# Performance work log

Measured on AMD Instinct MI355X. Metric: run time of the kernel, lower is better.

The kernel has to match this reference:

```python
import jax, jax.numpy as jnp
import numpy as np
import math

NEG_INF = -10000.0

def setup_inputs() -> dict:
    key = jax.random.key(0)
    k1, k2, k3 = jax.random.split(key, 3)
    B, Sq, Sk, H, D = 2, 2048, 2048, 16, 64
    q = jax.random.normal(k1, (B, Sq, H, D), dtype=jnp.float32)
    kv = jax.random.normal(k2, (B, Sk, 2, H, D), dtype=jnp.float32)
    key_padding_mask = jax.random.randint(k3, (B, Sk), 0, 2).astype(jnp.bool_)
    return {"q": q, "kv": kv, "key_padding_mask": key_padding_mask}

def reference(q, kv, key_padding_mask):
    # q: (B, Sq, H, D); kv: (B, Sk, 2, H, D); key_padding_mask: (B, Sk) True=keep
    D = q.shape[-1]
    softmax_scale = 1.0 / math.sqrt(D)
    k = kv[:, :, 0]  # (B, Sk, H, D)
    v = kv[:, :, 1]  # (B, Sk, H, D)
    # (B, H, Sq, Sk) score matrix
    scores = jnp.einsum('bthd,bshd->bhts', q, k * softmax_scale)
    # additive padding mask: 0 where keep, NEG_INF where masked out
    pad = jnp.where(key_padding_mask, 0.0, NEG_INF).astype(scores.dtype)
    scores = scores + pad[:, None, None, :]
    attention = jax.nn.softmax(scores, axis=-1)
    # dropout_p = 0.0 (eval mode) -> no-op
    output = jnp.einsum('bhts,bshd->bthd', attention, v)
    return output
```

## Files before the change

kernel.cpp:

```cpp
#include <hip/hip_runtime.h>

typedef unsigned short u16;
typedef unsigned int   u32;
typedef u16   u16x8 __attribute__((ext_vector_type(8)));
typedef float f32x4 __attribute__((ext_vector_type(4)));
typedef float f32x16 __attribute__((ext_vector_type(16)));
typedef __bf16 bf16x8 __attribute__((ext_vector_type(8)));
typedef u32   u32x4 __attribute__((ext_vector_type(4)));

#define QSCALE  0.18033688011112f
#define BM_OPEN  -28.8539008177793f
#define BM_MASK  -14455.8043097f

__device__ __forceinline__ u16 f2bf(float x){
  __bf16 h = (__bf16)x;
  return __builtin_bit_cast(u16, h);
}
__device__ __forceinline__ f32x16 mfma32(u16x8 a, u16x8 b, f32x16 c){
  return __builtin_amdgcn_mfma_f32_32x32x16_bf16(
      __builtin_bit_cast(bf16x8, a), __builtin_bit_cast(bf16x8, b), c, 0, 0, 0);
}
__device__ __forceinline__ void gld16(const void* g, void* l){
  __builtin_amdgcn_global_load_lds(
      (const __attribute__((address_space(1))) u32*)g,
      (__attribute__((address_space(3))) u32*)l, 16, 0, 0);
}
__device__ __forceinline__ u32 cvtpk(float lo, float hi){
  u32 d;
  asm("v_cvt_pk_bf16_f32 %0, %1, %2" : "=v"(d) : "v"(lo), "v"(hi));
  return d;
}
__device__ __forceinline__ void plswap(u32 &x, u32 &y){
  asm("v_permlane32_swap_b32 %0, %1" : "+v"(x), "+v"(y));
}


__global__ __launch_bounds__(256, 4)
void prepass(const float* __restrict__ KV, const int* __restrict__ MASK,
             u16* __restrict__ IMG, float* __restrict__ BIASM)
{
  const int tid = threadIdx.x;
  const int bid = blockIdx.x;
  const int kt = bid & 31;
  const int h  = (bid >> 5) & 15;
  const int b  = bid >> 9;
  const int kb = kt*64;
  const size_t kv_b = (size_t)b*(2048u*2048u);
  u16* tile = IMG + (size_t)bid * 8192;

  {
    const int skey = tid >> 2, scp = tid & 3;
    const float* kp = KV + kv_b + (size_t)(kb + skey)*2048 + h*64 + 16*scp;
    f32x4 f0 = *(const f32x4*)(kp);
    f32x4 f1 = *(const f32x4*)(kp + 4);
    f32x4 f2 = *(const f32x4*)(kp + 8);
    f32x4 f3 = *(const f32x4*)(kp + 12);
    u16x8 c0, c1;
    #pragma unroll
    for (int e = 0; e < 4; ++e){
      c0[e] = f2bf(f0[e]); c0[e+4] = f2bf(f1[e]);
      c1[e] = f2bf(f2[e]); c1[e+4] = f2bf(f3[e]);
    }
    const int idx0 = skey*64 + (((2*scp) ^ (skey & 7)) << 3);
    *(u16x8*)&tile[idx0]     = c0;
    *(u16x8*)&tile[idx0 ^ 8] = c1;
  }
  {
    const int sdb = tid & 7, ssp = tid >> 3;
    const float* vp = KV + kv_b + (size_t)(kb + 2*ssp)*2048 + 1024 + h*64 + 8*sdb;
    f32x4 r0a = *(const f32x4*)(vp);
    f32x4 r0b = *(const f32x4*)(vp + 4);
    f32x4 r1a = *(const f32x4*)(vp + 2048);
    f32x4 r1b = *(const f32x4*)(vp + 2048 + 4);
    u32* vimg = (u32*)(tile + 4096);
    const int wc = ssp >> 2, wi = ssp & 3;
    #pragma unroll
    for (int j = 0; j < 4; ++j){
      const int d0 = 8*sdb + j;
      const int d1 = d0 + 4;
      vimg[d0*32 + ((wc ^ (d0 & 7)) << 2) + wi] = (u32)f2bf(r0a[j]) | ((u32)f2bf(r1a[j]) << 16);
      vimg[d1*32 + ((wc ^ (d1 & 7)) << 2) + wi] = (u32)f2bf(r0b[j]) | ((u32)f2bf(r1b[j]) << 16);
    }
  }
  if (h == 0 && tid < 64){
    const int s = kb + tid;
    BIASM[b*2048 + s] = MASK[b*2048 + s] ? BM_OPEN : BM_MASK;
  }
}

template<int PRE>
__global__ __launch_bounds__(256, 3)
void attn_main(const float* __restrict__ Q, const float* __restrict__ KV,
               const int* __restrict__ MASK, const u16* __restrict__ IMG,
               const float* __restrict__ BIASM, float* __restrict__ OUT)
{
  __shared__ __align__(16) u16 KVbuf[2][8192];
  __shared__ __align__(16) float BiasLds[2048];

  const int tid  = threadIdx.x;
  const int lane = tid & 63;
  const int hi   = lane >> 5;
  const int lq   = lane & 31;

  const int bid0 = blockIdx.x;
  const int bid  = (bid0 & 7)*64 + (bid0 >> 3);
  const int qt  = bid & 15;
  const int h   = (bid >> 4) & 15;
  const int b   = bid >> 8;

  const int w    = tid >> 6;
  const int qbase = qt*128 + w*32;
  const size_t q_b  = (size_t)b * (2048u*1024u);
  const size_t kv_b = (size_t)b * (2048u*2048u);

  const int sw7 = lq & 7;

  u16x8 Qf[4];
  {
    const int qrow = qbase + lq;
    const float* qp = Q + q_b + (size_t)qrow*1024 + h*64 + 8*hi;
    #pragma unroll
    for (int kc = 0; kc < 4; ++kc){
      f32x4 a = *(const f32x4*)(qp + 16*kc);
      f32x4 c = *(const f32x4*)(qp + 16*kc + 4);
      u16x8 v;
      #pragma unroll
      for (int e = 0; e < 4; ++e){
        v[e]     = f2bf(a[e] * QSCALE);
        v[e + 4] = f2bf(c[e] * QSCALE);
      }
      Qf[kc] = v;
    }
  }

  f32x16 Oa[2];
  #pragma unroll
  for (int dt = 0; dt < 2; ++dt)
    #pragma unroll
    for (int r = 0; r < 16; ++r) Oa[dt][r] = 0.f;
  float lrun = 0.f;

  const char* img0 = (const char*)IMG + (size_t)((b*16 + h)*32) * 16384;
  const int so = tid*16;
  const int skey = tid >> 2, scp = tid & 3;
  const int sdb  = tid & 7,  ssp = tid >> 3;
  const float* kp0 = KV + kv_b + (size_t)skey*2048 + h*64 + 16*scp;
  const float* vp0 = KV + kv_b + (size_t)(2*ssp)*2048 + 1024 + h*64 + 8*sdb;
  f32x4 kf0, kf1, kf2, kf3, va, vb2, vc, vd;

#define STAGE_ISSUE(T, DST) do{                                               \
    const char* g_ = img0 + (size_t)(T)*16384;                                \
    char* l_ = (char*)(DST);                                                  \
    gld16(g_+so,        l_+so);                                               \
    gld16(g_+so+4096,   l_+so+4096);                                          \
    gld16(g_+so+8192,   l_+so+8192);                                          \
    gld16(g_+so+12288,  l_+so+12288);                                         \
  }while(0)

#define BIAS_STAGE() do{                                                      \
    const char* gb_ = (const char*)BIASM + (size_t)b*8192;                    \
    char* lb_ = (char*)BiasLds;                                               \
    gld16(gb_+so,      lb_+so);                                               \
    gld16(gb_+so+4096, lb_+so+4096);                                          \
  }while(0)

#define STAGE_REG(T) do{                                                      \
    const float* kp_ = kp0 + (size_t)(T)*64*2048;                             \
    kf0=*(const f32x4*)(kp_);   kf1=*(const f32x4*)(kp_+4);                   \
    kf2=*(const f32x4*)(kp_+8); kf3=*(const f32x4*)(kp_+12);                  \
    const float* vp_ = vp0 + (size_t)(T)*64*2048;                             \
    va=*(const f32x4*)(vp_);      vb2=*(const f32x4*)(vp_+4);                 \
    vc=*(const f32x4*)(vp_+2048); vd =*(const f32x4*)(vp_+2048+4);            \
  }while(0)

#define STAGE_WRITE(DST) do{                                                  \
    u16x8 c0_, c1_;                                                           \
    _Pragma("unroll") for (int e_=0; e_<4; ++e_){                             \
      c0_[e_]=f2bf(kf0[e_]); c0_[e_+4]=f2bf(kf1[e_]);                         \
      c1_[e_]=f2bf(kf2[e_]); c1_[e_+4]=f2bf(kf3[e_]); }                       \
    const int kix_ = skey*64 + (((2*scp) ^ (skey & 7)) << 3);                 \
    *(u16x8*)&(DST)[kix_]     = c0_;                                          \
    *(u16x8*)&(DST)[kix_ ^ 8] = c1_;                                          \
    u32* vimg_ = (u32*)((DST)+4096);                                          \
    const int wc_ = ssp >> 2, wi_ = ssp & 3;                                  \
    _Pragma("unroll") for (int j_=0; j_<4; ++j_){                             \
      const int d0_=8*sdb+j_, d1_=d0_+4;                                      \
      vimg_[d0_*32 + ((wc_ ^ (d0_&7)) << 2) + wi_] = (u32)f2bf(va[j_])  | ((u32)f2bf(vc[j_])<<16); \
      vimg_[d1_*32 + ((wc_ ^ (d1_&7)) << 2) + wi_] = (u32)f2bf(vb2[j_]) | ((u32)f2bf(vd[j_])<<16); \
    }                                                                         \
  }while(0)

#define COMPUTE(T, CUR) do{                                                   \
    const u16* Kb_ = (CUR);                                                   \
    const u32* vimg_ = (const u32*)((CUR) + 4096);                            \
    f32x16 S[2];                                                              \
    _Pragma("unroll") for (int ct = 0; ct < 2; ++ct){                         \
      _Pragma("unroll") for (int m = 0; m < 4; ++m){                          \
        f32x4 bq;                                                             \
        if constexpr (PRE){                                                   \
          bq = *(const f32x4*)&BiasLds[(T)*64 + 32*ct + 8*m + 4*hi];          \
        } else {                                                              \
          const int4 mv = *(const int4*)(MASK + b*2048 + (T)*64 + 32*ct + 8*m + 4*hi); \
          bq[0] = mv.x ? BM_OPEN : BM_MASK;                                   \
          bq[1] = mv.y ? BM_OPEN : BM_MASK;                                   \
          bq[2] = mv.z ? BM_OPEN : BM_MASK;                                   \
          bq[3] = mv.w ? BM_OPEN : BM_MASK;                                   \
        }                                                                     \
        S[ct][4*m+0] = bq[0]; S[ct][4*m+1] = bq[1];                           \
        S[ct][4*m+2] = bq[2]; S[ct][4*m+3] = bq[3];                           \
      }                                                                       \
    }                                                                         \
    __builtin_amdgcn_s_setprio(1);                                            \
    _Pragma("unroll") for (int ct = 0; ct < 2; ++ct){                         \
      _Pragma("unroll") for (int kc = 0; kc < 4; ++kc){                       \
        u16x8 kf = *(const u16x8*)&Kb_[(32*ct + lq)*64 + (((2*kc+hi)^sw7)<<3)]; \
        S[ct] = mfma32(kf, Qf[kc], S[ct]);                                    \
      }                                                                       \
    }                                                                         \
    __builtin_amdgcn_s_setprio(0);                                            \
    u32 pa[2][4], pb[2][4];                                                   \
    float ps = 0.f;                                                           \
    _Pragma("unroll") for (int ct = 0; ct < 2; ++ct){                         \
      _Pragma("unroll") for (int m = 0; m < 4; ++m){                          \
        const float p0 = __builtin_amdgcn_exp2f(S[ct][4*m+0]);                \
        const float p1 = __builtin_amdgcn_exp2f(S[ct][4*m+1]);                \
        const float p2 = __builtin_amdgcn_exp2f(S[ct][4*m+2]);                \
        const float p3 = __builtin_amdgcn_exp2f(S[ct][4*m+3]);                \
        ps += (p0 + p1) + (p2 + p3);                                          \
        pa[ct][m] = cvtpk(p0, p1);                                            \
        pb[ct][m] = cvtpk(p2, p3);                                            \
      }                                                                       \
    }                                                                         \
    lrun += ps;                                                               \
    u16x8 Pf[4];                                                              \
    _Pragma("unroll") for (int ct = 0; ct < 2; ++ct){                         \
      plswap(pa[ct][0], pa[ct][1]);  plswap(pb[ct][0], pb[ct][1]);            \
      plswap(pa[ct][2], pa[ct][3]);  plswap(pb[ct][2], pb[ct][3]);            \
      u32x4 f0_ = { pa[ct][0], pb[ct][0], pa[ct][1], pb[ct][1] };             \
      u32x4 f1_ = { pa[ct][2], pb[ct][2], pa[ct][3], pb[ct][3] };             \
      Pf[2*ct+0] = __builtin_bit_cast(u16x8, f0_);                            \
      Pf[2*ct+1] = __builtin_bit_cast(u16x8, f1_);                            \
    }                                                                         \
    __builtin_amdgcn_s_setprio(1);                                            \
    _Pragma("unroll") for (int dt = 0; dt < 2; ++dt){                         \
      _Pragma("unroll") for (int sc = 0; sc < 4; ++sc){                       \
        u32x4 vv = *(const u32x4*)&vimg_[(32*dt + lq)*32 + (((2*sc+hi)^sw7)<<2)]; \
        Oa[dt] = mfma32(__builtin_bit_cast(u16x8, vv), Pf[sc], Oa[dt]);       \
      }                                                                       \
    }                                                                         \
    __builtin_amdgcn_s_setprio(0);                                            \
  }while(0)

  if constexpr (PRE){
    BIAS_STAGE();
    STAGE_ISSUE(0, &KVbuf[0][0]);
  } else {
    STAGE_REG(0);
    STAGE_WRITE(&KVbuf[0][0]);
  }
  __syncthreads();

  for (int t = 0; t < 32; ++t){
    if (t < 31){
      if constexpr (PRE) STAGE_ISSUE(t+1, &KVbuf[(t+1) & 1][0]);
      else               STAGE_REG(t+1);
    }
    COMPUTE(t, &KVbuf[t & 1][0]);
    if (t < 31){
      if constexpr (!PRE) STAGE_WRITE(&KVbuf[(t+1) & 1][0]);
      __syncthreads();
    }
  }

  {
    float l_ = lrun + __shfl_xor(lrun, 32, 64);
    const float inv = 1.f / l_;
    const int qrow = qbase + lq;
    float* op = OUT + q_b + (size_t)qrow*1024 + h*64;
    #pragma unroll
    for (int dt = 0; dt < 2; ++dt){
      #pragma unroll
      for (int m = 0; m < 4; ++m){
        f32x4 ov;
        ov[0] = Oa[dt][4*m+0] * inv;
        ov[1] = Oa[dt][4*m+1] * inv;
        ov[2] = Oa[dt][4*m+2] * inv;
        ov[3] = Oa[dt][4*m+3] * inv;
        *(f32x4*)(op + 32*dt + 8*m + 4*hi) = ov;
      }
    }
  }
#undef STAGE_ISSUE
#undef BIAS_STAGE
#undef STAGE_REG
#undef STAGE_WRITE
#undef COMPUTE
}

extern "C" void kernel_launch(void* const* d_in, const int* in_sizes, int n_in,
                              void* d_out, int out_size, void* d_ws, size_t ws_size,
                              hipStream_t stream)
{
  const float* Q  = nullptr;
  const float* KV = nullptr;
  const int*   M  = nullptr;
  for (int i = 0; i < n_in; ++i){
    if      (in_sizes[i] == 4194304) Q  = (const float*)d_in[i];
    else if (in_sizes[i] == 8388608) KV = (const float*)d_in[i];
    else if (in_sizes[i] == 4096)    M  = (const int*)d_in[i];
  }
  if (!Q)  Q  = (const float*)d_in[0];
  if (!KV) KV = (const float*)d_in[1];
  if (!M)  M  = (const int*)d_in[2];
  float* O = (float*)d_out;

  const size_t NEED = 16384ull + 1024ull*16384ull;
  if (ws_size >= NEED){
    float* biasm = (float*)d_ws;
    u16*   img   = (u16*)((char*)d_ws + 16384);
    prepass<<<dim3(1024), dim3(256), 0, stream>>>(KV, M, img, biasm);
    attn_main<1><<<dim3(512), dim3(256), 0, stream>>>(Q, KV, M, img, biasm, O);
  } else {
    attn_main<0><<<dim3(512), dim3(256), 0, stream>>>(Q, KV, M, nullptr, nullptr, O);
  }
}
```

Before: 62.80 us.

## Process two KV tiles per iteration with dual accumulators and quad buffering

Measured after the change: 60.74 us. 1.03x faster.

```diff
diff --git a/kernel.cpp b/kernel.cpp
--- a/kernel.cpp
+++ b/kernel.cpp
@@ -89,12 +89,12 @@
 }
 
 template<int PRE>
-__global__ __launch_bounds__(256, 3)
+__global__ __launch_bounds__(256, 2)
 void attn_main(const float* __restrict__ Q, const float* __restrict__ KV,
                const int* __restrict__ MASK, const u16* __restrict__ IMG,
                const float* __restrict__ BIASM, float* __restrict__ OUT)
 {
-  __shared__ __align__(16) u16 KVbuf[2][8192];
+  __shared__ __align__(16) u16 KVbuf[4][8192];
   __shared__ __align__(16) float BiasLds[2048];
 
   const int tid  = threadIdx.x;
@@ -133,12 +133,12 @@
     }
   }
 
-  f32x16 Oa[2];
+  f32x16 Oa0[2], Oa1[2];
   #pragma unroll
   for (int dt = 0; dt < 2; ++dt)
     #pragma unroll
-    for (int r = 0; r < 16; ++r) Oa[dt][r] = 0.f;
-  float lrun = 0.f;
+    for (int r = 0; r < 16; ++r){ Oa0[dt][r] = 0.f; Oa1[dt][r] = 0.f; }
+  float lrun0 = 0.f, lrun1 = 0.f;
 
   const char* img0 = (const char*)IMG + (size_t)((b*16 + h)*32) * 16384;
   const int so = tid*16;
@@ -190,10 +190,7 @@
     }                                                                         \
   }while(0)
 
-#define COMPUTE(T, CUR) do{                                                   \
-    const u16* Kb_ = (CUR);                                                   \
-    const u32* vimg_ = (const u32*)((CUR) + 4096);                            \
-    f32x16 S[2];                                                              \
+#define SINIT(T, SD) do{                                                      \
     _Pragma("unroll") for (int ct = 0; ct < 2; ++ct){                         \
       _Pragma("unroll") for (int m = 0; m < 4; ++m){                          \
         f32x4 bq;                                                             \
@@ -206,74 +203,111 @@
           bq[2] = mv.z ? BM_OPEN : BM_MASK;                                   \
           bq[3] = mv.w ? BM_OPEN : BM_MASK;                                   \
         }                                                                     \
-        S[ct][4*m+0] = bq[0]; S[ct][4*m+1] = bq[1];                           \
-        S[ct][4*m+2] = bq[2]; S[ct][4*m+3] = bq[3];                           \
+        SD[ct][4*m+0] = bq[0]; SD[ct][4*m+1] = bq[1];                         \
+        SD[ct][4*m+2] = bq[2]; SD[ct][4*m+3] = bq[3];                         \
       }                                                                       \
     }                                                                         \
-    __builtin_amdgcn_s_setprio(1);                                            \
+  }while(0)
+
+#define QK(CUR, SD) do{                                                       \
+    const u16* Kb_ = (CUR);                                                   \
     _Pragma("unroll") for (int ct = 0; ct < 2; ++ct){                         \
       _Pragma("unroll") for (int kc = 0; kc < 4; ++kc){                       \
         u16x8 kf = *(const u16x8*)&Kb_[(32*ct + lq)*64 + (((2*kc+hi)^sw7)<<3)]; \
-        S[ct] = mfma32(kf, Qf[kc], S[ct]);                                    \
+        SD[ct] = mfma32(kf, Qf[kc], SD[ct]);                                  \
       }                                                                       \
     }                                                                         \
-    __builtin_amdgcn_s_setprio(0);                                            \
+  }while(0)
+
+#define SM(SD, PFD, LR) do{                                                   \
     u32 pa[2][4], pb[2][4];                                                   \
     float ps = 0.f;                                                           \
     _Pragma("unroll") for (int ct = 0; ct < 2; ++ct){                         \
       _Pragma("unroll") for (int m = 0; m < 4; ++m){                          \
-        const float p0 = __builtin_amdgcn_exp2f(S[ct][4*m+0]);                \
-        const float p1 = __builtin_amdgcn_exp2f(S[ct][4*m+1]);                \
-        const float p2 = __builtin_amdgcn_exp2f(S[ct][4*m+2]);                \
-        const float p3 = __builtin_amdgcn_exp2f(S[ct][4*m+3]);                \
+        const float p0 = __builtin_amdgcn_exp2f(SD[ct][4*m+0]);               \
+        const float p1 = __builtin_amdgcn_exp2f(SD[ct][4*m+1]);               \
+        const float p2 = __builtin_amdgcn_exp2f(SD[ct][4*m+2]);               \
+        const float p3 = __builtin_amdgcn_exp2f(SD[ct][4*m+3]);               \
         ps += (p0 + p1) + (p2 + p3);                                          \
         pa[ct][m] = cvtpk(p0, p1);                                            \
         pb[ct][m] = cvtpk(p2, p3);                                            \
       }                                                                       \
     }                                                                         \
-    lrun += ps;                                                               \
-    u16x8 Pf[4];                                                              \
+    LR += ps;                                                                 \
     _Pragma("unroll") for (int ct = 0; ct < 2; ++ct){                         \
       plswap(pa[ct][0], pa[ct][1]);  plswap(pb[ct][0], pb[ct][1]);            \
       plswap(pa[ct][2], pa[ct][3]);  plswap(pb[ct][2], pb[ct][3]);            \
       u32x4 f0_ = { pa[ct][0], pb[ct][0], pa[ct][1], pb[ct][1] };             \
       u32x4 f1_ = { pa[ct][2], pb[ct][2], pa[ct][3], pb[ct][3] };             \
-      Pf[2*ct+0] = __builtin_bit_cast(u16x8, f0_);                            \
-      Pf[2*ct+1] = __builtin_bit_cast(u16x8, f1_);                            \
-    }                                                                         \
-    __builtin_amdgcn_s_setprio(1);                                            \
+      PFD[2*ct+0] = __builtin_bit_cast(u16x8, f0_);                           \
+      PFD[2*ct+1] = __builtin_bit_cast(u16x8, f1_);                           \
+    }                                                                         \
+  }while(0)
+
+#define PV(CUR, PFD, OA) do{                                                  \
+    const u32* vimg_ = (const u32*)((CUR) + 4096);                            \
     _Pragma("unroll") for (int dt = 0; dt < 2; ++dt){                         \
       _Pragma("unroll") for (int sc = 0; sc < 4; ++sc){                       \
         u32x4 vv = *(const u32x4*)&vimg_[(32*dt + lq)*32 + (((2*sc+hi)^sw7)<<2)]; \
-        Oa[dt] = mfma32(__builtin_bit_cast(u16x8, vv), Pf[sc], Oa[dt]);       \
+        OA[dt] = mfma32(__builtin_bit_cast(u16x8, vv), PFD[sc], OA[dt]);      \
       }                                                                       \
     }                                                                         \
-    __builtin_amdgcn_s_setprio(0);                                            \
   }while(0)
 
   if constexpr (PRE){
     BIAS_STAGE();
     STAGE_ISSUE(0, &KVbuf[0][0]);
+    STAGE_ISSUE(1, &KVbuf[1][0]);
+    __syncthreads();
+
+    for (int u = 0; u < 16; ++u){
+      const int ps = (u & 1) << 1;
+      u16* ca = &KVbuf[0][0] + ps*8192;
+      u16* cb = ca + 8192;
+      if (u < 15){
+        u16* sa = &KVbuf[0][0] + (ps ^ 2)*8192;
+        STAGE_ISSUE(2*u + 2, sa);
+        STAGE_ISSUE(2*u + 3, sa + 8192);
+      }
+      f32x16 SA[2], SB[2];
+      u16x8 PfA[4], PfB[4];
+      SINIT(2*u,     SA);
+      SINIT(2*u + 1, SB);
+      __builtin_amdgcn_s_setprio(1);
+      QK(ca, SA);
+      QK(cb, SB);
+      __builtin_amdgcn_s_setprio(0);
+      SM(SA, PfA, lrun0);
+      SM(SB, PfB, lrun1);
+      __builtin_amdgcn_s_setprio(1);
+      PV(ca, PfA, Oa0);
+      PV(cb, PfB, Oa1);
+      __builtin_amdgcn_s_setprio(0);
+      if (u < 15) __syncthreads();
+    }
   } else {
     STAGE_REG(0);
     STAGE_WRITE(&KVbuf[0][0]);
-  }
-  __syncthreads();
-
-  for (int t = 0; t < 32; ++t){
-    if (t < 31){
-      if constexpr (PRE) STAGE_ISSUE(t+1, &KVbuf[(t+1) & 1][0]);
-      else               STAGE_REG(t+1);
-    }
-    COMPUTE(t, &KVbuf[t & 1][0]);
-    if (t < 31){
-      if constexpr (!PRE) STAGE_WRITE(&KVbuf[(t+1) & 1][0]);
-      __syncthreads();
+    __syncthreads();
+    for (int t = 0; t < 32; ++t){
+      if (t < 31) STAGE_REG(t+1);
+      u16* cur = &KVbuf[t & 1][0];
+      f32x16 SA[2];
+      u16x8 PfA[4];
+      SINIT(t, SA);
+      QK(cur, SA);
+      SM(SA, PfA, lrun0);
+      PV(cur, PfA, Oa0);
+      if (t < 31){
+        STAGE_WRITE(&KVbuf[(t+1) & 1][0]);
+        __syncthreads();
+      }
     }
   }
 
   {
-    float l_ = lrun + __shfl_xor(lrun, 32, 64);
+    const float lsum = lrun0 + lrun1;
+    const float l_ = lsum + __shfl_xor(lsum, 32, 64);
     const float inv = 1.f / l_;
     const int qrow = qbase + lq;
     float* op = OUT + q_b + (size_t)qrow*1024 + h*64;
@@ -282,10 +316,10 @@
       #pragma unroll
       for (int m = 0; m < 4; ++m){
         f32x4 ov;
-        ov[0] = Oa[dt][4*m+0] * inv;
-        ov[1] = Oa[dt][4*m+1] * inv;
-        ov[2] = Oa[dt][4*m+2] * inv;
-        ov[3] = Oa[dt][4*m+3] * inv;
+        ov[0] = (Oa0[dt][4*m+0] + Oa1[dt][4*m+0]) * inv;
+        ov[1] = (Oa0[dt][4*m+1] + Oa1[dt][4*m+1]) * inv;
+        ov[2] = (Oa0[dt][4*m+2] + Oa1[dt][4*m+2]) * inv;
+        ov[3] = (Oa0[dt][4*m+3] + Oa1[dt][4*m+3]) * inv;
         *(f32x4*)(op + 32*dt + 8*m + 4*hi) = ov;
       }
     }
@@ -294,7 +328,10 @@
 #undef BIAS_STAGE
 #undef STAGE_REG
 #undef STAGE_WRITE
-#undef COMPUTE
+#undef SINIT
+#undef QK
+#undef SM
+#undef PV
 }
 
 extern "C" void kernel_launch(void* const* d_in, const int* in_sizes, int n_in,
```

## Process two 32-row query subtiles per wave with 128-thread blocks

Applied to the files above, without the earlier changes.

New measurement: 89.05 us. 41.8% more time.

```diff
diff --git a/kernel.cpp b/kernel.cpp
--- a/kernel.cpp
+++ b/kernel.cpp
@@ -89,7 +89,7 @@
 }
 
 template<int PRE>
-__global__ __launch_bounds__(256, 3)
+__global__ __launch_bounds__(128, 2)
 void attn_main(const float* __restrict__ Q, const float* __restrict__ KV,
                const int* __restrict__ MASK, const u16* __restrict__ IMG,
                const float* __restrict__ BIASM, float* __restrict__ OUT)
@@ -101,6 +101,7 @@
   const int lane = tid & 63;
   const int hi   = lane >> 5;
   const int lq   = lane & 31;
+  const int w    = tid >> 6;
 
   const int bid0 = blockIdx.x;
   const int bid  = (bid0 & 7)*64 + (bid0 >> 3);
@@ -108,16 +109,17 @@
   const int h   = (bid >> 4) & 15;
   const int b   = bid >> 8;
 
-  const int w    = tid >> 6;
-  const int qbase = qt*128 + w*32;
+  const int qA = qt*128 + w*64;
+  const int qB = qA + 32;
   const size_t q_b  = (size_t)b * (2048u*1024u);
   const size_t kv_b = (size_t)b * (2048u*2048u);
 
   const int sw7 = lq & 7;
 
-  u16x8 Qf[4];
-  {
-    const int qrow = qbase + lq;
+  u16x8 QfA[4], QfB[4];
+  #pragma unroll
+  for (int st = 0; st < 2; ++st){
+    const int qrow = (st ? qB : qA) + lq;
     const float* qp = Q + q_b + (size_t)qrow*1024 + h*64 + 8*hi;
     #pragma unroll
     for (int kc = 0; kc < 4; ++kc){
@@ -129,71 +131,63 @@
         v[e]     = f2bf(a[e] * QSCALE);
         v[e + 4] = f2bf(c[e] * QSCALE);
       }
-      Qf[kc] = v;
-    }
-  }
-
-  f32x16 Oa[2];
+      if (st) QfB[kc] = v; else QfA[kc] = v;
+    }
+  }
+
+  f32x16 OaA[2], OaB[2];
   #pragma unroll
   for (int dt = 0; dt < 2; ++dt)
     #pragma unroll
-    for (int r = 0; r < 16; ++r) Oa[dt][r] = 0.f;
-  float lrun = 0.f;
+    for (int r = 0; r < 16; ++r){ OaA[dt][r] = 0.f; OaB[dt][r] = 0.f; }
+  float lrunA = 0.f, lrunB = 0.f;
 
   const char* img0 = (const char*)IMG + (size_t)((b*16 + h)*32) * 16384;
   const int so = tid*16;
-  const int skey = tid >> 2, scp = tid & 3;
-  const int sdb  = tid & 7,  ssp = tid >> 3;
-  const float* kp0 = KV + kv_b + (size_t)skey*2048 + h*64 + 16*scp;
-  const float* vp0 = KV + kv_b + (size_t)(2*ssp)*2048 + 1024 + h*64 + 8*sdb;
-  f32x4 kf0, kf1, kf2, kf3, va, vb2, vc, vd;
 
 #define STAGE_ISSUE(T, DST) do{                                               \
     const char* g_ = img0 + (size_t)(T)*16384;                                \
     char* l_ = (char*)(DST);                                                  \
-    gld16(g_+so,        l_+so);                                               \
-    gld16(g_+so+4096,   l_+so+4096);                                          \
-    gld16(g_+so+8192,   l_+so+8192);                                          \
-    gld16(g_+so+12288,  l_+so+12288);                                         \
+    _Pragma("unroll") for (int k_ = 0; k_ < 8; ++k_)                          \
+      gld16(g_ + so + 2048*k_, l_ + so + 2048*k_);                            \
   }while(0)
 
 #define BIAS_STAGE() do{                                                      \
     const char* gb_ = (const char*)BIASM + (size_t)b*8192;                    \
     char* lb_ = (char*)BiasLds;                                               \
-    gld16(gb_+so,      lb_+so);                                               \
-    gld16(gb_+so+4096, lb_+so+4096);                                          \
+    _Pragma("unroll") for (int k_ = 0; k_ < 4; ++k_)                          \
+      gld16(gb_ + so + 2048*k_, lb_ + so + 2048*k_);                          \
   }while(0)
 
-#define STAGE_REG(T) do{                                                      \
-    const float* kp_ = kp0 + (size_t)(T)*64*2048;                             \
-    kf0=*(const f32x4*)(kp_);   kf1=*(const f32x4*)(kp_+4);                   \
-    kf2=*(const f32x4*)(kp_+8); kf3=*(const f32x4*)(kp_+12);                  \
-    const float* vp_ = vp0 + (size_t)(T)*64*2048;                             \
-    va=*(const f32x4*)(vp_);      vb2=*(const f32x4*)(vp_+4);                 \
-    vc=*(const f32x4*)(vp_+2048); vd =*(const f32x4*)(vp_+2048+4);            \
-  }while(0)
-
-#define STAGE_WRITE(DST) do{                                                  \
-    u16x8 c0_, c1_;                                                           \
-    _Pragma("unroll") for (int e_=0; e_<4; ++e_){                             \
-      c0_[e_]=f2bf(kf0[e_]); c0_[e_+4]=f2bf(kf1[e_]);                         \
-      c1_[e_]=f2bf(kf2[e_]); c1_[e_+4]=f2bf(kf3[e_]); }                       \
-    const int kix_ = skey*64 + (((2*scp) ^ (skey & 7)) << 3);                 \
-    *(u16x8*)&(DST)[kix_]     = c0_;                                          \
-    *(u16x8*)&(DST)[kix_ ^ 8] = c1_;                                          \
-    u32* vimg_ = (u32*)((DST)+4096);                                          \
-    const int wc_ = ssp >> 2, wi_ = ssp & 3;                                  \
-    _Pragma("unroll") for (int j_=0; j_<4; ++j_){                             \
-      const int d0_=8*sdb+j_, d1_=d0_+4;                                      \
-      vimg_[d0_*32 + ((wc_ ^ (d0_&7)) << 2) + wi_] = (u32)f2bf(va[j_])  | ((u32)f2bf(vc[j_])<<16); \
-      vimg_[d1_*32 + ((wc_ ^ (d1_&7)) << 2) + wi_] = (u32)f2bf(vb2[j_]) | ((u32)f2bf(vd[j_])<<16); \
+#define SM(SD, PFD, LR) do{                                                   \
+    u32 pa[2][4], pb[2][4];                                                   \
+    float ps = 0.f;                                                           \
+    _Pragma("unroll") for (int ct = 0; ct < 2; ++ct){                         \
+      _Pragma("unroll") for (int m = 0; m < 4; ++m){                          \
+        const float p0 = __builtin_amdgcn_exp2f(SD[ct][4*m+0]);               \
+        const float p1 = __builtin_amdgcn_exp2f(SD[ct][4*m+1]);               \
+        const float p2 = __builtin_amdgcn_exp2f(SD[ct][4*m+2]);               \
+        const float p3 = __builtin_amdgcn_exp2f(SD[ct][4*m+3]);               \
+        ps += (p0 + p1) + (p2 + p3);                                          \
+        pa[ct][m] = cvtpk(p0, p1);                                            \
+        pb[ct][m] = cvtpk(p2, p3);                                            \
+      }                                                                       \
+    }                                                                         \
+    LR += ps;                                                                 \
+    _Pragma("unroll") for (int ct = 0; ct < 2; ++ct){                         \
+      plswap(pa[ct][0], pa[ct][1]);  plswap(pb[ct][0], pb[ct][1]);            \
+      plswap(pa[ct][2], pa[ct][3]);  plswap(pb[ct][2], pb[ct][3]);            \
+      u32x4 f0_ = { pa[ct][0], pb[ct][0], pa[ct][1], pb[ct][1] };             \
+      u32x4 f1_ = { pa[ct][2], pb[ct][2], pa[ct][3], pb[ct][3] };             \
+      PFD[2*ct+0] = __builtin_bit_cast(u16x8, f0_);                           \
+      PFD[2*ct+1] = __builtin_bit_cast(u16x8, f1_);                           \
     }                                                                         \
   }while(0)
 
 #define COMPUTE(T, CUR) do{                                                   \
     const u16* Kb_ = (CUR);                                                   \
     const u32* vimg_ = (const u32*)((CUR) + 4096);                            \
-    f32x16 S[2];                                                              \
+    f32x16 SA[2], SB[2];                                                      \
     _Pragma("unroll") for (int ct = 0; ct < 2; ++ct){                         \
       _Pragma("unroll") for (int m = 0; m < 4; ++m){                          \
         f32x4 bq;                                                             \
@@ -206,46 +200,31 @@
           bq[2] = mv.z ? BM_OPEN : BM_MASK;                                   \
           bq[3] = mv.w ? BM_OPEN : BM_MASK;                                   \
         }                                                                     \
-        S[ct][4*m+0] = bq[0]; S[ct][4*m+1] = bq[1];                           \
-        S[ct][4*m+2] = bq[2]; S[ct][4*m+3] = bq[3];                           \
+        SA[ct][4*m+0] = bq[0]; SA[ct][4*m+1] = bq[1];                         \
+        SA[ct][4*m+2] = bq[2]; SA[ct][4*m+3] = bq[3];                         \
+        SB[ct][4*m+0] = bq[0]; SB[ct][4*m+1] = bq[1];                         \
+        SB[ct][4*m+2] = bq[2]; SB[ct][4*m+3] = bq[3];                         \
       }                                                                       \
     }                                                                         \
     __builtin_amdgcn_s_setprio(1);                                            \
     _Pragma("unroll") for (int ct = 0; ct < 2; ++ct){                         \
       _Pragma("unroll") for (int kc = 0; kc < 4; ++kc){                       \
         u16x8 kf = *(const u16x8*)&Kb_[(32*ct + lq)*64 + (((2*kc+hi)^sw7)<<3)]; \
-        S[ct] = mfma32(kf, Qf[kc], S[ct]);                                    \
+        SA[ct] = mfma32(kf, QfA[kc], SA[ct]);                                 \
+        SB[ct] = mfma32(kf, QfB[kc], SB[ct]);                                 \
       }                                                                       \
     }                                                                         \
     __builtin_amdgcn_s_setprio(0);                                            \
-    u32 pa[2][4], pb[2][4];                                                   \
-    float ps = 0.f;                                                           \
-    _Pragma("unroll") for (int ct = 0; ct < 2; ++ct){                         \
-      _Pragma("unroll") for (int m = 0; m < 4; ++m){                          \
-        const float p0 = __builtin_amdgcn_exp2f(S[ct][4*m+0]);                \
-        const float p1 = __builtin_amdgcn_exp2f(S[ct][4*m+1]);                \
-        const float p2 = __builtin_amdgcn_exp2f(S[ct][4*m+2]);                \
-        const float p3 = __builtin_amdgcn_exp2f(S[ct][4*m+3]);                \
-        ps += (p0 + p1) + (p2 + p3);                                          \
-        pa[ct][m] = cvtpk(p0, p1);                                            \
-        pb[ct][m] = cvtpk(p2, p3);                                            \
-      }                                                                       \
-    }                                                                         \
-    lrun += ps;                                                               \
-    u16x8 Pf[4];                                                              \
-    _Pragma("unroll") for (int ct = 0; ct < 2; ++ct){                         \
-      plswap(pa[ct][0], pa[ct][1]);  plswap(pb[ct][0], pb[ct][1]);            \
-      plswap(pa[ct][2], pa[ct][3]);  plswap(pb[ct][2], pb[ct][3]);            \
-      u32x4 f0_ = { pa[ct][0], pb[ct][0], pa[ct][1], pb[ct][1] };             \
-      u32x4 f1_ = { pa[ct][2], pb[ct][2], pa[ct][3], pb[ct][3] };             \
-      Pf[2*ct+0] = __builtin_bit_cast(u16x8, f0_);                            \
-      Pf[2*ct+1] = __builtin_bit_cast(u16x8, f1_);                            \
-    }                                                                         \
+    u16x8 PfA[4], PfB[4];                                                     \
+    SM(SA, PfA, lrunA);                                                       \
+    SM(SB, PfB, lrunB);                                                       \
     __builtin_amdgcn_s_setprio(1);                                            \
     _Pragma("unroll") for (int dt = 0; dt < 2; ++dt){                         \
       _Pragma("unroll") for (int sc = 0; sc < 4; ++sc){                       \
         u32x4 vv = *(const u32x4*)&vimg_[(32*dt + lq)*32 + (((2*sc+hi)^sw7)<<2)]; \
-        Oa[dt] = mfma32(__builtin_bit_cast(u16x8, vv), Pf[sc], Oa[dt]);       \
+        u16x8 vf = __builtin_bit_cast(u16x8, vv);                             \
+        OaA[dt] = mfma32(vf, PfA[sc], OaA[dt]);                               \
+        OaB[dt] = mfma32(vf, PfB[sc], OaB[dt]);                               \
       }                                                                       \
     }                                                                         \
     __builtin_amdgcn_s_setprio(0);                                            \
@@ -255,45 +234,108 @@
     BIAS_STAGE();
     STAGE_ISSUE(0, &KVbuf[0][0]);
   } else {
-    STAGE_REG(0);
-    STAGE_WRITE(&KVbuf[0][0]);
+    const int row_ = tid >> 1, half_ = tid & 1;
+    const float* kp_ = KV + kv_b + (size_t)row_*2048 + h*64;
+    #pragma unroll
+    for (int cc = 0; cc < 4; ++cc){
+      const int c_ = 4*half_ + cc;
+      f32x4 fa = *(const f32x4*)(kp_ + 8*c_);
+      f32x4 fb = *(const f32x4*)(kp_ + 8*c_ + 4);
+      u16x8 cv;
+      #pragma unroll
+      for (int e = 0; e < 4; ++e){ cv[e] = f2bf(fa[e]); cv[e+4] = f2bf(fb[e]); }
+      *(u16x8*)&KVbuf[0][row_*64 + ((c_ ^ (row_ & 7)) << 3)] = cv;
+    }
+    const int sdb_ = tid & 7, sp0_ = (tid >> 3) & 15;
+    u32* vimg_ = (u32*)&KVbuf[0][4096];
+    #pragma unroll
+    for (int rep = 0; rep < 2; ++rep){
+      const int ssp_ = sp0_ + 16*rep;
+      const float* vp_ = KV + kv_b + (size_t)(2*ssp_)*2048 + 1024 + h*64 + 8*sdb_;
+      f32x4 va = *(const f32x4*)(vp_);
+      f32x4 vb2 = *(const f32x4*)(vp_ + 4);
+      f32x4 vc = *(const f32x4*)(vp_ + 2048);
+      f32x4 vd = *(const f32x4*)(vp_ + 2048 + 4);
+      const int wc_ = ssp_ >> 2, wi_ = ssp_ & 3;
+      #pragma unroll
+      for (int j = 0; j < 4; ++j){
+        const int d0_ = 8*sdb_ + j, d1_ = d0_ + 4;
+        vimg_[d0_*32 + ((wc_ ^ (d0_&7)) << 2) + wi_] = (u32)f2bf(va[j])  | ((u32)f2bf(vc[j]) << 16);
+        vimg_[d1_*32 + ((wc_ ^ (d1_&7)) << 2) + wi_] = (u32)f2bf(vb2[j]) | ((u32)f2bf(vd[j]) << 16);
+      }
+    }
   }
   __syncthreads();
 
   for (int t = 0; t < 32; ++t){
-    if (t < 31){
-      if constexpr (PRE) STAGE_ISSUE(t+1, &KVbuf[(t+1) & 1][0]);
-      else               STAGE_REG(t+1);
-    }
-    COMPUTE(t, &KVbuf[t & 1][0]);
-    if (t < 31){
-      if constexpr (!PRE) STAGE_WRITE(&KVbuf[(t+1) & 1][0]);
-      __syncthreads();
-    }
-  }
-
-  {
-    float l_ = lrun + __shfl_xor(lrun, 32, 64);
+    if constexpr (PRE){
+      if (t < 31) STAGE_ISSUE(t+1, &KVbuf[(t+1) & 1][0]);
+      COMPUTE(t, &KVbuf[t & 1][0]);
+      if (t < 31) __syncthreads();
+    } else {
+      COMPUTE(t, &KVbuf[0][0]);
+      if (t < 31){
+        __syncthreads();
+        const int kb_ = (t+1)*64;
+        const int row_ = tid >> 1, half_ = tid & 1;
+        const float* kp_ = KV + kv_b + (size_t)(kb_ + row_)*2048 + h*64;
+        #pragma unroll
+        for (int cc = 0; cc < 4; ++cc){
+          const int c_ = 4*half_ + cc;
+          f32x4 fa = *(const f32x4*)(kp_ + 8*c_);
+          f32x4 fb = *(const f32x4*)(kp_ + 8*c_ + 4);
+          u16x8 cv;
+          #pragma unroll
+          for (int e = 0; e < 4; ++e){ cv[e] = f2bf(fa[e]); cv[e+4] = f2bf(fb[e]); }
+          *(u16x8*)&KVbuf[0][row_*64 + ((c_ ^ (row_ & 7)) << 3)] = cv;
+        }
+        const int sdb_ = tid & 7, sp0_ = (tid >> 3) & 15;
+        u32* vimg_ = (u32*)&KVbuf[0][4096];
+        #pragma unroll
+        for (int rep = 0; rep < 2; ++rep){
+          const int ssp_ = sp0_ + 16*rep;
+          const float* vp_ = KV + kv_b + (size_t)(kb_ + 2*ssp_)*2048 + 1024 + h*64 + 8*sdb_;
+          f32x4 va = *(const f32x4*)(vp_);
+          f32x4 vb2 = *(const f32x4*)(vp_ + 4);
+          f32x4 vc = *(const f32x4*)(vp_ + 2048);
+          f32x4 vd = *(const f32x4*)(vp_ + 2048 + 4);
+          const int wc_ = ssp_ >> 2, wi_ = ssp_ & 3;
+          #pragma unroll
+          for (int j = 0; j < 4; ++j){
+            const int d0_ = 8*sdb_ + j, d1_ = d0_ + 4;
+            vimg_[d0_*32 + ((wc_ ^ (d0_&7)) << 2) + wi_] = (u32)f2bf(va[j])  | ((u32)f2bf(vc[j]) << 16);
+            vimg_[d1_*32 + ((wc_ ^ (d1_&7)) << 2) + wi_] = (u32)f2bf(vb2[j]) | ((u32)f2bf(vd[j]) << 16);
+          }
+        }
+        __syncthreads();
+      }
+    }
+  }
+
+  #pragma unroll
+  for (int st = 0; st < 2; ++st){
+    const float lr = st ? lrunB : lrunA;
+    const float l_ = lr + __shfl_xor(lr, 32, 64);
     const float inv = 1.f / l_;
-    const int qrow = qbase + lq;
+    const int qrow = (st ? qB : qA) + lq;
     float* op = OUT + q_b + (size_t)qrow*1024 + h*64;
     #pragma unroll
     for (int dt = 0; dt < 2; ++dt){
       #pragma unroll
       for (int m = 0; m < 4; ++m){
         f32x4 ov;
-        ov[0] = Oa[dt][4*m+0] * inv;
-        ov[1] = Oa[dt][4*m+1] * inv;
-        ov[2] = Oa[dt][4*m+2] * inv;
-        ov[3] = Oa[dt][4*m+3] * inv;
+        const f32x16& Od = st ? OaB[dt] : OaA[dt];
+        ov[0] = Od[4*m+0] * inv;
+        ov[1] = Od[4*m+1] * inv;
+        ov[2] = Od[4*m+2] * inv;
+        ov[3] = Od[4*m+3] * inv;
         *(f32x4*)(op + 32*dt + 8*m + 4*hi) = ov;
       }
     }
   }
 #undef STAGE_ISSUE
 #undef BIAS_STAGE
-#undef STAGE_REG
-#undef STAGE_WRITE
+#undef SM
 #undef COMPUTE
 }
 
@@ -319,8 +361,8 @@
     float* biasm = (float*)d_ws;
     u16*   img   = (u16*)((char*)d_ws + 16384);
     prepass<<<dim3(1024), dim3(256), 0, stream>>>(KV, M, img, biasm);
-    attn_main<1><<<dim3(512), dim3(256), 0, stream>>>(Q, KV, M, img, biasm, O);
+    attn_main<1><<<dim3(512), dim3(128), 0, stream>>>(Q, KV, M, img, biasm, O);
   } else {
-    attn_main<0><<<dim3(512), dim3(256), 0, stream>>>(Q, KV, M, nullptr, nullptr, O);
-  }
-}
+    attn_main<0><<<dim3(512), dim3(128), 0, stream>>>(Q, KV, M, nullptr, nullptr, O);
+  }
+}
```
